# Kernel tuning notes

Measured on AMD Instinct MI355X. Metric: run time of the kernel, lower is better.

Reference implementation:

```python
import jax, jax.numpy as jnp
import numpy as np

EMB_DIM = 512
CATE1_CNT = 10
VOCAB = 100000
H_D = 1024
BN_EPS = 1e-5
NEG = -1e30  # masked value for max-pool


def setup_inputs() -> dict:
    key = jax.random.key(0)
    ks = jax.random.split(key, 12)
    B, LT, LD = 1024, 50, 200
    title = jax.random.randint(ks[0], (B, LT), 0, VOCAB, dtype=jnp.int64)
    desc = jax.random.randint(ks[1], (B, LD), 0, VOCAB, dtype=jnp.int64)
    t_len = jax.random.randint(ks[2], (B,), 1, LT + 1, dtype=jnp.int64)
    d_len = jax.random.randint(ks[3], (B,), 1, LD + 1, dtype=jnp.int64)
    emb = jax.random.normal(ks[4], (VOCAB, EMB_DIM), dtype=jnp.float32) * 0.02
    W_fc = jax.random.normal(ks[5], (4 * EMB_DIM, H_D), dtype=jnp.float32) * (1.0 / np.sqrt(4 * EMB_DIM))
    b_fc = jnp.zeros((H_D,), dtype=jnp.float32)
    gamma = jnp.ones((H_D,), dtype=jnp.float32)
    beta = jnp.zeros((H_D,), dtype=jnp.float32)
    W_clf = jax.random.normal(ks[6], (H_D, CATE1_CNT), dtype=jnp.float32) * (1.0 / np.sqrt(H_D))
    b_clf = jnp.zeros((CATE1_CNT,), dtype=jnp.float32)
    return {"title": title, "desc": desc, "t_len": t_len, "d_len": d_len,
            "emb": emb, "W_fc": W_fc, "b_fc": b_fc, "gamma": gamma,
            "beta": beta, "W_clf": W_clf, "b_clf": b_clf}


def _swem_pool(tokens, lens, emb):
    # tokens: [B, L] int, lens: [B] int -> (avg, max) each [B, D]
    e = emb[tokens]                                   # [B, L, D] gather
    L = tokens.shape[1]
    mask = (jnp.arange(L)[None, :] < lens[:, None])[..., None]  # [B, L, 1]
    s = jnp.sum(jnp.where(mask, e, 0.0), axis=1)      # [B, D]
    avg = s / jnp.maximum(lens, 1).astype(e.dtype)[:, None]
    mx = jnp.max(jnp.where(mask, e, NEG), axis=1)     # [B, D]
    return avg, mx


def reference(title, desc, t_len, d_len, emb, W_fc, b_fc, gamma, beta, W_clf, b_clf):
    t_avg, t_max = _swem_pool(title, t_len, emb)
    d_avg, d_max = _swem_pool(desc, d_len, emb)
    swem = jnp.concatenate([t_avg, t_max, d_avg, d_max], axis=-1)  # [B, 2048]
    h = swem @ W_fc + b_fc                                         # [B, H_D]
    # BatchNorm1d in training mode: batch statistics
    mean = jnp.mean(h, axis=0)
    var = jnp.var(h, axis=0)
    h = (h - mean) * jax.lax.rsqrt(var + BN_EPS) * gamma + beta
    h = jax.nn.relu(h)
    return h @ W_clf + b_clf                                       # [B, 10]
```

## Files before the change

kernel.cpp:

```cpp
#include <hip/hip_runtime.h>
#include <hip/hip_bf16.h>

#define EMB_DIM 512
#define B_SZ 1024
#define LT 50
#define LD 200
#define H_D 1024
#define K_FC 2048
#define NCLS 10
#define BN_EPS 1e-5f
#define NEGV -1e30f

typedef short short8 __attribute__((ext_vector_type(8)));
typedef float f32x4 __attribute__((ext_vector_type(4)));

#define SWZ(r, b) ((b) ^ (((r) & 7) << 4))

#define ACC4(S, M, E) \
  S.x += E.x; S.y += E.y; S.z += E.z; S.w += E.w; \
  M.x = fmaxf(M.x, E.x); M.y = fmaxf(M.y, E.y); \
  M.z = fmaxf(M.z, E.z); M.w = fmaxf(M.w, E.w);

__global__ __launch_bounds__(512) void pool_tr_kernel(
    const int* __restrict__ title, const int* __restrict__ desc,
    const int* __restrict__ t_len, const int* __restrict__ d_len,
    const float* __restrict__ emb, __hip_bfloat16* __restrict__ swem,
    const float* __restrict__ W, __hip_bfloat16* __restrict__ Wt,
    const float* __restrict__ Wclf, float* __restrict__ WclfT) {
  __shared__ float sm[8192];
  __shared__ int idxs[264];

  const int bid = blockIdx.x;
  const int tid = threadIdx.x;

  if (bid >= 2 * B_SZ) {
    const int t = bid - 2 * B_SZ;
    if (t == 512) {
      for (int idx = tid; idx < NCLS * H_D; idx += 512) {
        int j = idx >> 10, k = idx & 1023;
        WclfT[j * H_D + k] = Wclf[(size_t)k * NCLS + j];
      }
      return;
    }
    const int n0 = (t & 15) * 64;
    const int k0 = (t >> 4) * 64;
#pragma unroll
    for (int i = 0; i < 8; ++i) {
      int idx = i * 512 + tid;
      int r = idx >> 6, c = idx & 63;
      sm[r * 65 + c] = W[(size_t)(k0 + r) * H_D + n0 + c];
    }
    __syncthreads();
#pragma unroll
    for (int i = 0; i < 8; ++i) {
      int idx = i * 512 + tid;
      int r = idx >> 6, c = idx & 63;
      Wt[(size_t)(n0 + r) * K_FC + k0 + c] = __float2bfloat16(sm[c * 65 + r]);
    }
    return;
  }

  const int b = bid >> 1;
  const int half = bid & 1;
  const int wave = tid >> 6;
  const int lane = tid & 63;
  const int dbase = half * 256 + lane * 4;

  if (tid < LT) idxs[tid] = title[b * LT + tid];
  else if (tid >= 64 && tid < 64 + LD) idxs[tid] = desc[b * LD + tid - 64];
  const int tl = t_len[b];
  const int dl = d_len[b];
  __syncthreads();

#define POOL_LIST(LEN, IDXOFF, SARR, MARR)                                         \
  {                                                                                \
    float4 s0 = make_float4(0.f, 0.f, 0.f, 0.f), s1 = s0;                          \
    float4 m0 = make_float4(NEGV, NEGV, NEGV, NEGV), m1 = m0;                      \
    const int cnt = (LEN > wave) ? ((LEN - wave + 7) >> 3) : 0;                    \
    if (cnt >= 2) {                                                                \
      float4 e0 = *reinterpret_cast<const float4*>(                                \
          emb + (size_t)idxs[IDXOFF + wave] * EMB_DIM + dbase);                    \
      float4 e1 = *reinterpret_cast<const float4*>(                                \
          emb + (size_t)idxs[IDXOFF + wave + 8] * EMB_DIM + dbase);                \
      int i = 2;                                                                   \
      for (; i + 1 < cnt; i += 2) {                                                \
        float4 n0 = *reinterpret_cast<const float4*>(                              \
            emb + (size_t)idxs[IDXOFF + wave + i * 8] * EMB_DIM + dbase);          \
        float4 n1 = *reinterpret_cast<const float4*>(                              \
            emb + (size_t)idxs[IDXOFF + wave + (i + 1) * 8] * EMB_DIM + dbase);    \
        ACC4(s0, m0, e0); ACC4(s1, m1, e1);                                        \
        e0 = n0; e1 = n1;                                                          \
      }                                                                            \
      ACC4(s0, m0, e0); ACC4(s1, m1, e1);                                          \
      if (i < cnt) {                                                               \
        float4 t2 = *reinterpret_cast<const float4*>(                              \
            emb + (size_t)idxs[IDXOFF + wave + i * 8] * EMB_DIM + dbase);          \
        ACC4(s0, m0, t2);                                                          \
      }                                                                            \
    } else if (cnt == 1) {                                                         \
      float4 e0 = *reinterpret_cast<const float4*>(                                \
          emb + (size_t)idxs[IDXOFF + wave] * EMB_DIM + dbase);                    \
      ACC4(s0, m0, e0);                                                            \
    }                                                                              \
    s0.x += s1.x; s0.y += s1.y; s0.z += s1.z; s0.w += s1.w;                        \
    m0.x = fmaxf(m0.x, m1.x); m0.y = fmaxf(m0.y, m1.y);                            \
    m0.z = fmaxf(m0.z, m1.z); m0.w = fmaxf(m0.w, m1.w);                            \
    *reinterpret_cast<float4*>(&sm[(SARR * 8 + wave) * 256 + lane * 4]) = s0;      \
    *reinterpret_cast<float4*>(&sm[(MARR * 8 + wave) * 256 + lane * 4]) = m0;      \
  }

  POOL_LIST(tl, 0, 0, 1)
  POOL_LIST(dl, 64, 2, 3)

  __syncthreads();

  if (tid < 64) {
    const float it = 1.0f / (float)tl;
    const float id = 1.0f / (float)dl;
    float4 ts = make_float4(0.f, 0.f, 0.f, 0.f);
    float4 tm = make_float4(NEGV, NEGV, NEGV, NEGV);
    float4 ds = make_float4(0.f, 0.f, 0.f, 0.f);
    float4 dm = make_float4(NEGV, NEGV, NEGV, NEGV);
#pragma unroll
    for (int w = 0; w < 8; ++w) {
      float4 a = *reinterpret_cast<const float4*>(&sm[(0 * 8 + w) * 256 + tid * 4]);
      ts.x += a.x; ts.y += a.y; ts.z += a.z; ts.w += a.w;
      float4 bmx = *reinterpret_cast<const float4*>(&sm[(1 * 8 + w) * 256 + tid * 4]);
      tm.x = fmaxf(tm.x, bmx.x); tm.y = fmaxf(tm.y, bmx.y);
      tm.z = fmaxf(tm.z, bmx.z); tm.w = fmaxf(tm.w, bmx.w);
      float4 c = *reinterpret_cast<const float4*>(&sm[(2 * 8 + w) * 256 + tid * 4]);
      ds.x += c.x; ds.y += c.y; ds.z += c.z; ds.w += c.w;
      float4 dmx = *reinterpret_cast<const float4*>(&sm[(3 * 8 + w) * 256 + tid * 4]);
      dm.x = fmaxf(dm.x, dmx.x); dm.y = fmaxf(dm.y, dmx.y);
      dm.z = fmaxf(dm.z, dmx.z); dm.w = fmaxf(dm.w, dmx.w);
    }
    __hip_bfloat16* row = swem + (size_t)b * K_FC + half * 256 + tid * 4;
    union { ushort4 v; __hip_bfloat16 h[4]; } u;
    u.h[0] = __float2bfloat16(ts.x * it); u.h[1] = __float2bfloat16(ts.y * it);
    u.h[2] = __float2bfloat16(ts.z * it); u.h[3] = __float2bfloat16(ts.w * it);
    *reinterpret_cast<ushort4*>(&row[0 * EMB_DIM]) = u.v;
    u.h[0] = __float2bfloat16(tm.x); u.h[1] = __float2bfloat16(tm.y);
    u.h[2] = __float2bfloat16(tm.z); u.h[3] = __float2bfloat16(tm.w);
    *reinterpret_cast<ushort4*>(&row[1 * EMB_DIM]) = u.v;
    u.h[0] = __float2bfloat16(ds.x * id); u.h[1] = __float2bfloat16(ds.y * id);
    u.h[2] = __float2bfloat16(ds.z * id); u.h[3] = __float2bfloat16(ds.w * id);
    *reinterpret_cast<ushort4*>(&row[2 * EMB_DIM]) = u.v;
    u.h[0] = __float2bfloat16(dm.x); u.h[1] = __float2bfloat16(dm.y);
    u.h[2] = __float2bfloat16(dm.z); u.h[3] = __float2bfloat16(dm.w);
    *reinterpret_cast<ushort4*>(&row[3 * EMB_DIM]) = u.v;
  }
}

__global__ __launch_bounds__(256) void gemm_mfma_kernel(
    const __hip_bfloat16* __restrict__ A,
    const __hip_bfloat16* __restrict__ Bt,
    const float* __restrict__ bias, float* __restrict__ C,
    float* __restrict__ psum, float* __restrict__ psq) {
  __shared__ unsigned char As[8192];
  __shared__ unsigned char Bs[8192];
  __shared__ float reds[2][2][2][16];
  __shared__ float redq[2][2][2][16];
  const int tid = threadIdx.x;
  const int lane = tid & 63;
  const int wave = tid >> 6;
  const int wr = wave >> 1, wc = wave & 1;
  const int m0 = blockIdx.y * 64, n0 = blockIdx.x * 64;

  f32x4 acc[2][2] = {};

  const int c0 = tid * 2, c1 = tid * 2 + 1;
  const int r0s = c0 >> 3, o0 = c0 & 7;
  const int r1s = c1 >> 3, o1 = c1 & 7;
  const int hi = lane >> 4;
  const int lo = lane & 15;

  const __hip_bfloat16* pa0 = A + (size_t)(m0 + r0s) * K_FC + o0 * 8;
  const __hip_bfloat16* pa1 = A + (size_t)(m0 + r1s) * K_FC + o1 * 8;
  const __hip_bfloat16* pb0 = Bt + (size_t)(n0 + r0s) * K_FC + o0 * 8;
  const __hip_bfloat16* pb1 = Bt + (size_t)(n0 + r1s) * K_FC + o1 * 8;

  float4 a0 = *reinterpret_cast<const float4*>(pa0);
  float4 a1 = *reinterpret_cast<const float4*>(pa1);
  float4 b0 = *reinterpret_cast<const float4*>(pb0);
  float4 b1 = *reinterpret_cast<const float4*>(pb1);

  for (int k0 = 0; k0 < K_FC; k0 += 64) {
    __syncthreads();
    *reinterpret_cast<float4*>(As + SWZ(r0s, r0s * 128 + o0 * 16)) = a0;
    *reinterpret_cast<float4*>(As + SWZ(r1s, r1s * 128 + o1 * 16)) = a1;
    *reinterpret_cast<float4*>(Bs + SWZ(r0s, r0s * 128 + o0 * 16)) = b0;
    *reinterpret_cast<float4*>(Bs + SWZ(r1s, r1s * 128 + o1 * 16)) = b1;
    __syncthreads();

    if (k0 + 64 < K_FC) {
      a0 = *reinterpret_cast<const float4*>(pa0 + k0 + 64);
      a1 = *reinterpret_cast<const float4*>(pa1 + k0 + 64);
      b0 = *reinterpret_cast<const float4*>(pb0 + k0 + 64);
      b1 = *reinterpret_cast<const float4*>(pb1 + k0 + 64);
    }

#pragma unroll
    for (int kks = 0; kks < 2; ++kks) {
      short8 af[2], bfr[2];
#pragma unroll
      for (int mi = 0; mi < 2; ++mi) {
        int r = wr * 32 + mi * 16 + lo;
        af[mi] = *reinterpret_cast<const short8*>(As + SWZ(r, r * 128 + kks * 64 + hi * 16));
      }
#pragma unroll
      for (int ni = 0; ni < 2; ++ni) {
        int r = wc * 32 + ni * 16 + lo;
        bfr[ni] = *reinterpret_cast<const short8*>(Bs + SWZ(r, r * 128 + kks * 64 + hi * 16));
      }
#pragma unroll
      for (int mi = 0; mi < 2; ++mi)
#pragma unroll
        for (int ni = 0; ni < 2; ++ni)
          acc[mi][ni] = __builtin_amdgcn_mfma_f32_16x16x32_bf16(af[mi], bfr[ni], acc[mi][ni], 0, 0, 0);
    }
  }

#pragma unroll
  for (int ni = 0; ni < 2; ++ni) {
    int col = n0 + wc * 32 + ni * 16 + lo;
    float bv = bias[col];
    float s = 0.f, q = 0.f;
#pragma unroll
    for (int mi = 0; mi < 2; ++mi) {
#pragma unroll
      for (int r = 0; r < 4; ++r) {
        float v = acc[mi][ni][r] + bv;
        s += v; q += v * v;
        int rowm = m0 + wr * 32 + mi * 16 + hi * 4 + r;
        C[(size_t)rowm * H_D + col] = v;
      }
    }
    s += __shfl_xor(s, 16);
    s += __shfl_xor(s, 32);
    q += __shfl_xor(q, 16);
    q += __shfl_xor(q, 32);
    if (lane < 16) { reds[wr][wc][ni][lo] = s; redq[wr][wc][ni][lo] = q; }
  }
  __syncthreads();
  if (tid < 64) {
    int wc2 = tid >> 5, ni2 = (tid >> 4) & 1, lo2 = tid & 15;
    float s = reds[0][wc2][ni2][lo2] + reds[1][wc2][ni2][lo2];
    float q = redq[0][wc2][ni2][lo2] + redq[1][wc2][ni2][lo2];
    psum[blockIdx.y * H_D + n0 + tid] = s;
    psq[blockIdx.y * H_D + n0 + tid] = q;
  }
}

__global__ __launch_bounds__(256) void bn_final_kernel(
    const float* __restrict__ psum, const float* __restrict__ psq,
    const float* __restrict__ gamma, const float* __restrict__ beta,
    float* __restrict__ scale, float* __restrict__ shift) {
  const int col = blockIdx.x * 256 + threadIdx.x;
  float s = 0.f, q = 0.f;
#pragma unroll
  for (int i = 0; i < 16; ++i) {
    s += psum[i * H_D + col];
    q += psq[i * H_D + col];
  }
  const float inv_n = 1.0f / (float)B_SZ;
  float mean = s * inv_n;
  float var = q * inv_n - mean * mean;
  float rstd = rsqrtf(var + BN_EPS);
  float sc = rstd * gamma[col];
  scale[col] = sc;
  shift[col] = beta[col] - mean * sc;
}

__global__ __launch_bounds__(256) void clf_kernel(
    const float* __restrict__ h, const float* __restrict__ scale,
    const float* __restrict__ shift, const float* __restrict__ WT,
    const float* __restrict__ bclf, float* __restrict__ out) {
  __shared__ float v[H_D];
  const int row = blockIdx.x;
  const int tid = threadIdx.x;
#pragma unroll
  for (int i = 0; i < 4; ++i) {
    int k = tid + i * 256;
    float x = h[(size_t)row * H_D + k] * scale[k] + shift[k];
    v[k] = fmaxf(x, 0.f);
  }
  __syncthreads();
  const int wave = tid >> 6, lane = tid & 63;
  for (int j = wave; j < NCLS; j += 4) {
    const float* wrow = WT + j * H_D;
    float acc = 0.f;
#pragma unroll
    for (int i = 0; i < 16; ++i) {
      int k = lane + i * 64;
      acc += v[k] * wrow[k];
    }
#pragma unroll
    for (int off = 32; off > 0; off >>= 1) acc += __shfl_down(acc, off, 64);
    if (lane == 0) out[(size_t)row * NCLS + j] = acc + bclf[j];
  }
}

extern "C" void kernel_launch(void* const* d_in, const int* in_sizes, int n_in,
                              void* d_out, int out_size, void* d_ws, size_t ws_size,
                              hipStream_t stream) {
  const int* title = (const int*)d_in[0];
  const int* desc  = (const int*)d_in[1];
  const int* t_len = (const int*)d_in[2];
  const int* d_len = (const int*)d_in[3];
  const float* emb   = (const float*)d_in[4];
  const float* W_fc  = (const float*)d_in[5];
  const float* b_fc  = (const float*)d_in[6];
  const float* gamma = (const float*)d_in[7];
  const float* beta  = (const float*)d_in[8];
  const float* W_clf = (const float*)d_in[9];
  const float* b_clf = (const float*)d_in[10];
  float* out = (float*)d_out;

  unsigned char* ws = (unsigned char*)d_ws;
  __hip_bfloat16* swem = (__hip_bfloat16*)ws;
  __hip_bfloat16* Wt   = (__hip_bfloat16*)(ws + (4u << 20));
  float* h     = (float*)(ws + (8u << 20));
  float* psum  = (float*)(ws + (12u << 20));
  float* psq   = psum + 16 * H_D;
  float* scale = psq + 16 * H_D;
  float* shift = scale + H_D;
  float* WclfT = shift + H_D;

  const int n_tr_blocks = (K_FC / 64) * (H_D / 64) + 1;
  pool_tr_kernel<<<2 * B_SZ + n_tr_blocks, 512, 0, stream>>>(
      title, desc, t_len, d_len, emb, swem, W_fc, Wt, W_clf, WclfT);
  gemm_mfma_kernel<<<dim3(H_D / 64, B_SZ / 64), 256, 0, stream>>>(swem, Wt, b_fc, h, psum, psq);
  bn_final_kernel<<<H_D / 256, 256, 0, stream>>>(psum, psq, gamma, beta, scale, shift);
  clf_kernel<<<B_SZ, 256, 0, stream>>>(h, scale, shift, WclfT, b_clf, out);
}
```

Measured before the change: 74.29 us.

## Double-buffer GEMM LDS tiles and use 8 waves per block

The FC GEMM now uses 512 threads (8 waves in a 2x4 layout), and each wave computes a 32x16 output slice instead of 32x32. Shared-memory A/B tiles are double-buffered with register prefetch two k-steps ahead, which removes one barrier per iteration. The aim is more latency hiding and overlap of global loads with MFMA work. In exchange, the block uses twice the LDS and loads the A fragments redundantly across the extra waves.

```diff
diff --git a/kernel.cpp b/kernel.cpp
--- a/kernel.cpp
+++ b/kernel.cpp
@@ -151,85 +151,82 @@
   }
 }
 
-__global__ __launch_bounds__(256) void gemm_mfma_kernel(
+__global__ __launch_bounds__(512) void gemm_mfma_kernel(
     const __hip_bfloat16* __restrict__ A,
     const __hip_bfloat16* __restrict__ Bt,
     const float* __restrict__ bias, float* __restrict__ C,
     float* __restrict__ psum, float* __restrict__ psq) {
-  __shared__ unsigned char As[8192];
-  __shared__ unsigned char Bs[8192];
-  __shared__ float reds[2][2][2][16];
-  __shared__ float redq[2][2][2][16];
+  __shared__ unsigned char As[2][8192];
+  __shared__ unsigned char Bs[2][8192];
+  __shared__ float reds[2][4][16];
+  __shared__ float redq[2][4][16];
   const int tid = threadIdx.x;
   const int lane = tid & 63;
   const int wave = tid >> 6;
-  const int wr = wave >> 1, wc = wave & 1;
+  const int wr = wave >> 2;
+  const int wc = wave & 3;
   const int m0 = blockIdx.y * 64, n0 = blockIdx.x * 64;
 
-  f32x4 acc[2][2] = {};
-
-  const int c0 = tid * 2, c1 = tid * 2 + 1;
-  const int r0s = c0 >> 3, o0 = c0 & 7;
-  const int r1s = c1 >> 3, o1 = c1 & 7;
+  f32x4 acc[2] = {};
+
+  const int rs = tid >> 3;
+  const int os = tid & 7;
   const int hi = lane >> 4;
   const int lo = lane & 15;
 
-  const __hip_bfloat16* pa0 = A + (size_t)(m0 + r0s) * K_FC + o0 * 8;
-  const __hip_bfloat16* pa1 = A + (size_t)(m0 + r1s) * K_FC + o1 * 8;
-  const __hip_bfloat16* pb0 = Bt + (size_t)(n0 + r0s) * K_FC + o0 * 8;
-  const __hip_bfloat16* pb1 = Bt + (size_t)(n0 + r1s) * K_FC + o1 * 8;
-
-  float4 a0 = *reinterpret_cast<const float4*>(pa0);
-  float4 a1 = *reinterpret_cast<const float4*>(pa1);
-  float4 b0 = *reinterpret_cast<const float4*>(pb0);
-  float4 b1 = *reinterpret_cast<const float4*>(pb1);
-
+  const __hip_bfloat16* pa = A + (size_t)(m0 + rs) * K_FC + os * 8;
+  const __hip_bfloat16* pb = Bt + (size_t)(n0 + rs) * K_FC + os * 8;
+  const int swz = SWZ(rs, rs * 128 + os * 16);
+
+  float4 a1 = *reinterpret_cast<const float4*>(pa);
+  float4 b1 = *reinterpret_cast<const float4*>(pb);
+  *reinterpret_cast<float4*>(&As[0][swz]) = a1;
+  *reinterpret_cast<float4*>(&Bs[0][swz]) = b1;
+  a1 = *reinterpret_cast<const float4*>(pa + 64);
+  b1 = *reinterpret_cast<const float4*>(pb + 64);
+  __syncthreads();
+
+  int cur = 0;
   for (int k0 = 0; k0 < K_FC; k0 += 64) {
-    __syncthreads();
-    *reinterpret_cast<float4*>(As + SWZ(r0s, r0s * 128 + o0 * 16)) = a0;
-    *reinterpret_cast<float4*>(As + SWZ(r1s, r1s * 128 + o1 * 16)) = a1;
-    *reinterpret_cast<float4*>(Bs + SWZ(r0s, r0s * 128 + o0 * 16)) = b0;
-    *reinterpret_cast<float4*>(Bs + SWZ(r1s, r1s * 128 + o1 * 16)) = b1;
-    __syncthreads();
-
-    if (k0 + 64 < K_FC) {
-      a0 = *reinterpret_cast<const float4*>(pa0 + k0 + 64);
-      a1 = *reinterpret_cast<const float4*>(pa1 + k0 + 64);
-      b0 = *reinterpret_cast<const float4*>(pb0 + k0 + 64);
-      b1 = *reinterpret_cast<const float4*>(pb1 + k0 + 64);
+    float4 an = make_float4(0.f, 0.f, 0.f, 0.f), bn = an;
+    if (k0 + 128 < K_FC) {
+      an = *reinterpret_cast<const float4*>(pa + k0 + 128);
+      bn = *reinterpret_cast<const float4*>(pb + k0 + 128);
     }
 
 #pragma unroll
     for (int kks = 0; kks < 2; ++kks) {
-      short8 af[2], bfr[2];
+      short8 af[2];
 #pragma unroll
       for (int mi = 0; mi < 2; ++mi) {
         int r = wr * 32 + mi * 16 + lo;
-        af[mi] = *reinterpret_cast<const short8*>(As + SWZ(r, r * 128 + kks * 64 + hi * 16));
+        af[mi] = *reinterpret_cast<const short8*>(&As[cur][SWZ(r, r * 128 + kks * 64 + hi * 16)]);
       }
-#pragma unroll
-      for (int ni = 0; ni < 2; ++ni) {
-        int r = wc * 32 + ni * 16 + lo;
-        bfr[ni] = *reinterpret_cast<const short8*>(Bs + SWZ(r, r * 128 + kks * 64 + hi * 16));
-      }
+      int rb = wc * 16 + lo;
+      short8 bf = *reinterpret_cast<const short8*>(&Bs[cur][SWZ(rb, rb * 128 + kks * 64 + hi * 16)]);
 #pragma unroll
       for (int mi = 0; mi < 2; ++mi)
-#pragma unroll
-        for (int ni = 0; ni < 2; ++ni)
-          acc[mi][ni] = __builtin_amdgcn_mfma_f32_16x16x32_bf16(af[mi], bfr[ni], acc[mi][ni], 0, 0, 0);
-    }
-  }
-
-#pragma unroll
-  for (int ni = 0; ni < 2; ++ni) {
-    int col = n0 + wc * 32 + ni * 16 + lo;
+        acc[mi] = __builtin_amdgcn_mfma_f32_16x16x32_bf16(af[mi], bf, acc[mi], 0, 0, 0);
+    }
+
+    if (k0 + 64 < K_FC) {
+      *reinterpret_cast<float4*>(&As[cur ^ 1][swz]) = a1;
+      *reinterpret_cast<float4*>(&Bs[cur ^ 1][swz]) = b1;
+    }
+    __syncthreads();
+    a1 = an; b1 = bn;
+    cur ^= 1;
+  }
+
+  {
+    int col = n0 + wc * 16 + lo;
     float bv = bias[col];
     float s = 0.f, q = 0.f;
 #pragma unroll
     for (int mi = 0; mi < 2; ++mi) {
 #pragma unroll
       for (int r = 0; r < 4; ++r) {
-        float v = acc[mi][ni][r] + bv;
+        float v = acc[mi][r] + bv;
         s += v; q += v * v;
         int rowm = m0 + wr * 32 + mi * 16 + hi * 4 + r;
         C[(size_t)rowm * H_D + col] = v;
@@ -239,13 +236,13 @@
     s += __shfl_xor(s, 32);
     q += __shfl_xor(q, 16);
     q += __shfl_xor(q, 32);
-    if (lane < 16) { reds[wr][wc][ni][lo] = s; redq[wr][wc][ni][lo] = q; }
+    if (lane < 16) { reds[wr][wc][lo] = s; redq[wr][wc][lo] = q; }
   }
   __syncthreads();
   if (tid < 64) {
-    int wc2 = tid >> 5, ni2 = (tid >> 4) & 1, lo2 = tid & 15;
-    float s = reds[0][wc2][ni2][lo2] + reds[1][wc2][ni2][lo2];
-    float q = redq[0][wc2][ni2][lo2] + redq[1][wc2][ni2][lo2];
+    int wc2 = tid >> 4, lo2 = tid & 15;
+    float s = reds[0][wc2][lo2] + reds[1][wc2][lo2];
+    float q = redq[0][wc2][lo2] + redq[1][wc2][lo2];
     psum[blockIdx.y * H_D + n0 + tid] = s;
     psq[blockIdx.y * H_D + n0 + tid] = q;
   }
@@ -329,7 +326,7 @@
   const int n_tr_blocks = (K_FC / 64) * (H_D / 64) + 1;
   pool_tr_kernel<<<2 * B_SZ + n_tr_blocks, 512, 0, stream>>>(
       title, desc, t_len, d_len, emb, swem, W_fc, Wt, W_clf, WclfT);
-  gemm_mfma_kernel<<<dim3(H_D / 64, B_SZ / 64), 256, 0, stream>>>(swem, Wt, b_fc, h, psum, psq);
+  gemm_mfma_kernel<<<dim3(H_D / 64, B_SZ / 64), 512, 0, stream>>>(swem, Wt, b_fc, h, psum, psq);
   bn_final_kernel<<<H_D / 256, 256, 0, stream>>>(psum, psq, gamma, beta, scale, shift);
   clf_kernel<<<B_SZ, 256, 0, stream>>>(h, scale, shift, WclfT, b_clf, out);
 }
```

New measurement: 64.31 us. 13.4% less time.
